# Kernel optimization log

Measured on AMD Instinct MI355X. Metric: run time of the kernel, lower is better.

The kernel has to match this reference:

```python
import jax, jax.numpy as jnp
from jax import lax
import numpy as np

K = 10            # size_feat
N_MU = 10         # number of mean-PSF components
NCH = K * K + N_MU  # 110 depthwise channels
KLEN = 65         # precomputed kernel length


def setup_inputs() -> dict:
    key = jax.random.key(0)
    ks = jax.random.split(key, 12)
    B, C, H, W = 1, 3, 256, 256
    img = jax.random.uniform(ks[0], (B, C, H, W), jnp.float32)
    zernike = jax.random.normal(ks[1], (B, H, W, 35), jnp.float32)
    # pos displacements (first 2 channels) scaled to a few pixels
    zernike = zernike.at[..., :2].multiply(2.0)
    fc1_w = jax.random.normal(ks[2], (200, 33), jnp.float32) / np.float32(np.sqrt(33))
    fc1_b = jax.random.normal(ks[3], (200,), jnp.float32) * 0.01
    fc2_w = jax.random.normal(ks[4], (200, 200), jnp.float32) / np.float32(np.sqrt(200))
    fc2_b = jax.random.normal(ks[5], (200,), jnp.float32) * 0.01
    fc3_w = jax.random.normal(ks[6], (100, 200), jnp.float32) * 0.01
    fc3_b = jnp.zeros((100,), jnp.float32)
    basis_left = jax.random.normal(ks[7], (KLEN, K), jnp.float32) * 0.05
    basis_right = jax.random.normal(ks[8], (KLEN, K), jnp.float32) * 0.05
    mu = jax.random.uniform(ks[9], (KLEN, N_MU), jnp.float32) / np.float32(KLEN)
    return dict(img=img, zernike=zernike, fc1_w=fc1_w, fc1_b=fc1_b,
                fc2_w=fc2_w, fc2_b=fc2_b, fc3_w=fc3_w, fc3_b=fc3_b,
                basis_left=basis_left, basis_right=basis_right, mu=mu, ksize=65)


def _grid_sample_border(img, pos):
    """Bilinear grid_sample, padding_mode='border', align_corners=False.
    img: (B,C,H,W), pos: (B,H,W,2) pixel displacements (x,y)."""
    B, C, H, W = img.shape
    yy, xx = jnp.meshgrid(jnp.arange(H, dtype=jnp.float32),
                          jnp.arange(W, dtype=jnp.float32), indexing='ij')
    grid = jnp.stack((xx, yy), -1)                       # (H,W,2)
    wh = jnp.array([W - 1, H - 1], jnp.float32)
    flow = 2.0 * (grid[None] + pos) / wh - 1.0           # (B,H,W,2) in [-1,1]
    ix = ((flow[..., 0] + 1.0) * W - 1.0) * 0.5
    iy = ((flow[..., 1] + 1.0) * H - 1.0) * 0.5
    ix = jnp.clip(ix, 0.0, W - 1)
    iy = jnp.clip(iy, 0.0, H - 1)
    x0 = jnp.floor(ix); y0 = jnp.floor(iy)
    wx = ix - x0;       wy = iy - y0
    x0i = jnp.clip(x0.astype(jnp.int32), 0, W - 1)
    y0i = jnp.clip(y0.astype(jnp.int32), 0, H - 1)
    x1i = jnp.clip(x0i + 1, 0, W - 1)
    y1i = jnp.clip(y0i + 1, 0, H - 1)

    def bilerp(im, x0i, x1i, y0i, y1i, wx, wy):
        g = lambda yi, xi: im[:, yi, xi]                 # (C,H,W)
        top = g(y0i, x0i) * (1 - wx) + g(y0i, x1i) * wx
        bot = g(y1i, x0i) * (1 - wx) + g(y1i, x1i) * wx
        return top * (1 - wy) + bot * wy

    return jax.vmap(bilerp)(img, x0i, x1i, y0i, y1i, wx, wy)


def _depthwise(x, w, pad_axis, pad):
    # x: (N, NCH, H, W); w: (NCH,1,kh,kw). Reflect 'same' padding on pad_axis.
    cfg = [(0, 0)] * 4
    cfg[pad_axis] = (pad, pad)
    xp = jnp.pad(x, cfg, mode='reflect')
    return lax.conv_general_dilated(
        xp, w, (1, 1), 'VALID',
        dimension_numbers=('NCHW', 'OIHW', 'NCHW'),
        feature_group_count=x.shape[1])


def _forward(img, zernike, fc1_w, fc1_b, fc2_w, fc2_b, fc3_w, fc3_b,
             basis_left, basis_right, mu, ksize):
    B, C, H, W = img.shape
    pad = ksize // 2
    # --- grid-sample warp ---
    tilt = _grid_sample_border(img, zernike[..., :2])    # (B,C,H,W)
    # --- per-pixel MLP -> PSF coefficients ---
    f = zernike[..., 2:]                                  # (B,H,W,33)
    h = jax.nn.leaky_relu(f @ fc1_w.T + fc1_b)
    h = jax.nn.leaky_relu(h @ fc2_w.T + fc2_b)
    coef = h @ fc3_w.T + fc3_b                            # (B,H,W,100)
    weight = jnp.concatenate(
        [coef, jnp.ones((B, H, W, N_MU), coef.dtype)], -1)  # (B,H,W,110)
    # --- elementwise weight multiply ---
    big = jnp.concatenate([tilt, jnp.ones_like(tilt)], 1)  # (B,2C,H,W)
    big = big[..., None] * weight[:, None]                 # (B,2C,H,W,110)
    x = big.reshape(B * 2 * C, H, W, NCH).transpose(0, 3, 1, 2)  # (B*2C,110,H,W)
    # --- separable depthwise blur kernels (outer products Z_i x X_j + mu) ---
    wl = jnp.concatenate([jnp.repeat(basis_left.T, K, axis=0), mu.T], 0)  # (110,klen)
    wr = jnp.concatenate([jnp.tile(basis_right.T, (K, 1)), mu.T], 0)      # (110,klen)
    wl = wl[:, None, :, None]                              # (110,1,klen,1)
    wr = wr[:, None, None, :]                              # (110,1,1,klen)
    y = _depthwise(x, wl, 2, pad)
    y = _depthwise(y, wr, 3, pad)
    d = y.reshape(B, 2 * C, NCH, H, W)
    out = jnp.sum(d[:, :3], axis=2) / jnp.sum(d[:, 3:], axis=2)  # (B,3,H,W)
    return out


def reference(img, zernike, fc1_w, fc1_b, fc2_w, fc2_b, fc3_w, fc3_b,
              basis_left, basis_right, mu, ksize):
    return _forward(img, zernike, fc1_w, fc1_b, fc2_w, fc2_b, fc3_w, fc3_b,
                    basis_left, basis_right, mu, ksize)
```

## Files before the change

kernel.cpp:

```cpp
#include <hip/hip_runtime.h>

#define HW 65536

typedef __attribute__((ext_vector_type(8))) short short8;
typedef __attribute__((ext_vector_type(4))) float float4v;

__device__ __forceinline__ int refl(int i){ if (i < 0) i = -i; if (i > 255) i = 510 - i; return i; }
__device__ __forceinline__ float lrelu(float x){ return x > 0.f ? x : 0.01f * x; }
__device__ __forceinline__ unsigned int f2bf(float x){
  union { float f; unsigned int u; } v; v.f = x;
  unsigned int r = v.u + 0x7fff + ((v.u >> 16) & 1);
  return r >> 16;
}
__device__ __forceinline__ unsigned int pk_bf16(float lo, float hi){
  unsigned int r;
  asm("v_cvt_pk_bf16_f32 %0, %1, %2" : "=v"(r) : "v"(lo), "v"(hi));
  return r;
}
__device__ __forceinline__ unsigned short f2h(float x){
  union { _Float16 h; unsigned short u; } v; v.h = (_Float16)x; return v.u;
}
__device__ __forceinline__ float h2f(unsigned short u){
  union { _Float16 h; unsigned short u; } v; v.u = u; return (float)v.h;
}

#define W2OFF 13312
#define W3OFF 59904
__global__ __launch_bounds__(256) void k_prep(const float* __restrict__ w1,
    const float* __restrict__ w2, const float* __restrict__ w3,
    const float* __restrict__ bl, const float* __restrict__ br,
    const float* __restrict__ mu, unsigned short* __restrict__ wbf,
    unsigned short* __restrict__ Tt, float* __restrict__ mucp){
  __shared__ float sm[650];
  __shared__ float sq[10];
  int bid = blockIdx.x;
  int tid = threadIdx.x;
  if (bid < 512){
    int i = bid * 256 + tid;
    if (i < 84992){
      if (i < 208 * 64){
        int n = i >> 6, k = i & 63;
        float v = (n < 200 && k < 33) ? w1[n * 33 + k] : 0.f;
        wbf[i] = (unsigned short)f2bf(v);
      } else if (i < W2OFF + 208 * 224){
        int j = i - W2OFF; int n = j / 224, k = j - n * 224;
        float v = (n < 200 && k < 200) ? w2[n * 200 + k] : 0.f;
        wbf[i] = (unsigned short)f2bf(v);
      } else {
        int j = i - W3OFF; int n = j / 224, k = j - n * 224;
        float v = (n < 100 && k < 200) ? w3[n * 200 + k] : 0.f;
        wbf[i] = (unsigned short)f2bf(v);
      }
    } else {
      int e = i - 84992;
      int t = e / 1536, rem = e - t * 1536;
      int m = rem / 96, k = rem - m * 96;
      int d = k - m;
      float v = 0.f;
      if (d >= 0 && d <= 64){
        if (t < 10)      v = bl[d * 10 + t];
        else if (t < 20) v = mu[d * 10 + (t - 10)];
        else             v = br[d * 10 + (t - 20)];
      }
      Tt[e] = (unsigned short)f2bf(v);
    }
  } else {
    for (int e = tid; e < 650; e += 256) sm[e] = mu[e];
    __syncthreads();
    if (tid < 10){
      float s = 0.f;
      for (int u = 0; u < 65; ++u) s += sm[u * 10 + tid];
      sq[tid] = s * s;
    }
    __syncthreads();
    if (tid == 0){
      float m = 0.f;
      #pragma unroll
      for (int mm = 0; mm < 10; ++mm) m += sq[mm];
      mucp[0] = m;
    }
  }
}

#define HSTR 232
#define BUFB 14848
__global__ __launch_bounds__(512) void k_mlp(const float* __restrict__ img,
    const float* __restrict__ zern,
    const float* __restrict__ b1f, const float* __restrict__ b2f,
    const float* __restrict__ b3f, const unsigned short* __restrict__ wbf,
    float* __restrict__ tilt, unsigned short* __restrict__ coefb){
  __shared__ char smem[2 * BUFB];
  unsigned short* H1  = (unsigned short*)smem;
  unsigned short* H3u = (unsigned short*)smem;
  unsigned short* XB  = (unsigned short*)(smem + BUFB);
  unsigned short* H2  = XB;
  int tid = threadIdx.x;
  int pix0 = blockIdx.x * 32;
  int lane = tid & 63, wv = tid >> 6;
  int ln = lane & 15, qd = lane >> 4;

  if (tid < 96){
    int m = tid & 31, c = tid >> 5;
    int pix = pix0 + m;
    int x = pix & 255, y = pix >> 8;
    float px = zern[pix * 35 + 0], py = zern[pix * 35 + 1];
    float ix = ((float)x + px) * (256.f / 255.f) - 0.5f;
    float iy = ((float)y + py) * (256.f / 255.f) - 0.5f;
    ix = fminf(fmaxf(ix, 0.f), 255.f);
    iy = fminf(fmaxf(iy, 0.f), 255.f);
    float x0f = floorf(ix), y0f = floorf(iy);
    float wx = ix - x0f, wy = iy - y0f;
    int x0 = (int)x0f, y0 = (int)y0f;
    int x1 = min(x0 + 1, 255), y1 = min(y0 + 1, 255);
    const float* im = img + c * HW;
    float g00 = im[y0 * 256 + x0], g01 = im[y0 * 256 + x1];
    float g10 = im[y1 * 256 + x0], g11 = im[y1 * 256 + x1];
    float top = g00 * (1.f - wx) + g01 * wx;
    float bot = g10 * (1.f - wx) + g11 * wx;
    tilt[c * HW + pix] = top * (1.f - wy) + bot * wy;
  }

  for (int e = tid; e < 1152; e += 512) ((int*)XB)[e] = 0;
  for (int e = tid; e < 384; e += 512){
    int m = e / 12, j = e - m * 12;
    ((int*)H1)[m * 116 + 104 + j] = 0;
  }
  __syncthreads();
  for (int e = tid; e < 32 * 33; e += 512){
    int m = e / 33, k = e - m * 33;
    XB[m * 72 + k] = (unsigned short)f2bf(zern[(pix0 + m) * 35 + 2 + k]);
  }
  __syncthreads();

  for (int nt = wv; nt < 13; nt += 8){
    int n = nt * 16 + ln;
    short8 b0 = *(const short8*)(wbf + n * 64 + qd * 8);
    short8 b1 = *(const short8*)(wbf + n * 64 + 32 + qd * 8);
    float bv = (n < 200) ? b1f[n] : 0.f;
    #pragma unroll
    for (int mt = 0; mt < 2; ++mt){
      float4v acc = {bv, bv, bv, bv};
      short8 a0 = *(const short8*)(XB + (mt * 16 + ln) * 72 + qd * 8);
      short8 a1 = *(const short8*)(XB + (mt * 16 + ln) * 72 + 32 + qd * 8);
      acc = __builtin_amdgcn_mfma_f32_16x16x32_bf16(a0, b0, acc, 0, 0, 0);
      acc = __builtin_amdgcn_mfma_f32_16x16x32_bf16(a1, b1, acc, 0, 0, 0);
      #pragma unroll
      for (int r = 0; r < 4; ++r)
        H1[(mt * 16 + qd * 4 + r) * HSTR + n] = (unsigned short)f2bf(lrelu(acc[r]));
    }
  }
  __syncthreads();

  for (int e = tid; e < 384; e += 512){
    int m = e / 12, j = e - m * 12;
    ((int*)H2)[m * 116 + 104 + j] = 0;
  }
  {
    const unsigned short* w2p = wbf + W2OFF;
    for (int nt = wv; nt < 13; nt += 8){
      int n = nt * 16 + ln;
      short8 bf[7];
      #pragma unroll
      for (int kc = 0; kc < 7; ++kc)
        bf[kc] = *(const short8*)(w2p + n * 224 + kc * 32 + qd * 8);
      float bv = (n < 200) ? b2f[n] : 0.f;
      #pragma unroll
      for (int mt = 0; mt < 2; ++mt){
        float4v acc = {bv, bv, bv, bv};
        #pragma unroll
        for (int kc = 0; kc < 7; ++kc){
          short8 af = *(const short8*)(H1 + (mt * 16 + ln) * HSTR + kc * 32 + qd * 8);
          acc = __builtin_amdgcn_mfma_f32_16x16x32_bf16(af, bf[kc], acc, 0, 0, 0);
        }
        #pragma unroll
        for (int r = 0; r < 4; ++r)
          H2[(mt * 16 + qd * 4 + r) * HSTR + n] = (unsigned short)f2bf(lrelu(acc[r]));
      }
    }
  }
  __syncthreads();

  {
    const unsigned short* w3p = wbf + W3OFF;
    for (int nt = wv; nt < 7; nt += 8){
      int n = nt * 16 + ln;
      short8 bf[7];
      #pragma unroll
      for (int kc = 0; kc < 7; ++kc)
        bf[kc] = *(const short8*)(w3p + n * 224 + kc * 32 + qd * 8);
      float bv = (n < 100) ? b3f[n] : 0.f;
      #pragma unroll
      for (int mt = 0; mt < 2; ++mt){
        float4v acc = {bv, bv, bv, bv};
        #pragma unroll
        for (int kc = 0; kc < 7; ++kc){
          short8 af = *(const short8*)(H2 + (mt * 16 + ln) * HSTR + kc * 32 + qd * 8);
          acc = __builtin_amdgcn_mfma_f32_16x16x32_bf16(af, bf[kc], acc, 0, 0, 0);
        }
        #pragma unroll
        for (int r = 0; r < 4; ++r)
          H3u[(mt * 16 + qd * 4 + r) * 113 + n] = f2h(acc[r]);
      }
    }
  }
  __syncthreads();

  for (int e = tid; e < 1600; e += 512){
    int n = e >> 4, mp = e & 15;
    unsigned int lo = H3u[(2 * mp) * 113 + n];
    unsigned int hi = H3u[(2 * mp + 1) * 113 + n];
    *(unsigned int*)(coefb + n * HW + pix0 + 2 * mp) = lo | (hi << 16);
  }
}

#define VB 344
__global__ __launch_bounds__(256) void k_vconv16(const float* __restrict__ tilt,
    const unsigned short* __restrict__ coefb, const unsigned short* __restrict__ Tt,
    unsigned short* __restrict__ sbuf, unsigned short* __restrict__ smu){
  __shared__ __align__(16) unsigned short sxb[2][16 * VB];
  int tid = threadIdx.x;
  int bid = blockIdx.x;
  int lane = tid & 63, wv = tid >> 6;
  int ln = lane & 15, qd = lane >> 4;
  int col = tid & 15, seg = tid >> 4;
  int r0 = seg * 20;

  int goff[20];
  #pragma unroll
  for (int q = 0; q < 20; ++q) goff[q] = refl(r0 + q - 32) * 256 + col;

  for (int e = tid; e < 768; e += 256){
    int b = e / 384, r = e - b * 384;
    int cc = r / 24, rp = r - cc * 24;
    sxb[b][cc * VB + 320 + rp] = 0;
  }

  if (bid < 640){
    int s = bid & 15;
    int cj = bid >> 4;
    int c = cj / 10, j = cj - c * 10;
    int x0 = s * 16;
    float treg[20];
    if (c < 3){
      const float* tc = tilt + c * HW + x0;
      #pragma unroll
      for (int q = 0; q < 20; ++q) treg[q] = tc[goff[q]];
    }
    unsigned short pf[20];
    {
      const unsigned short* cq = coefb + j * HW + x0;
      #pragma unroll
      for (int q = 0; q < 20; ++q) pf[q] = cq[goff[q]];
    }
    float4v acc[4];
    #pragma unroll
    for (int t = 0; t < 4; ++t) acc[t] = (float4v){0.f, 0.f, 0.f, 0.f};
    for (int i = 0; i < 10; ++i){
      int us = i & 1;
      unsigned short* sb = sxb[us];
      if (c < 3){
        #pragma unroll
        for (int q = 0; q < 10; ++q){
          float v0 = h2f(pf[2 * q]) * treg[2 * q];
          float v1 = h2f(pf[2 * q + 1]) * treg[2 * q + 1];
          *(unsigned int*)&sb[col * VB + r0 + 2 * q] = pk_bf16(v0, v1);
        }
      } else {
        #pragma unroll
        for (int q = 0; q < 10; ++q){
          *(unsigned int*)&sb[col * VB + r0 + 2 * q] = pk_bf16(h2f(pf[2 * q]), h2f(pf[2 * q + 1]));
        }
      }
      __syncthreads();
      if (i < 9){
        const unsigned short* cn = coefb + ((i + 1) * 10 + j) * HW + x0;
        #pragma unroll
        for (int q = 0; q < 20; ++q) pf[q] = cn[goff[q]];
      }
      const unsigned short* ta = Tt + i * 1536 + ln * 96 + qd * 8;
      short8 A0 = *(const short8*)(ta);
      short8 A1 = *(const short8*)(ta + 32);
      short8 A2 = *(const short8*)(ta + 64);
      #pragma unroll
      for (int t = 0; t < 4; ++t){
        int yt = wv * 4 + t;
        const unsigned short* bp = sb + ln * VB + yt * 16 + qd * 8;
        short8 B0 = *(const short8*)(bp);
        short8 B1 = *(const short8*)(bp + 32);
        short8 B2 = *(const short8*)(bp + 64);
        acc[t] = __builtin_amdgcn_mfma_f32_16x16x32_bf16(A0, B0, acc[t], 0, 0, 0);
        acc[t] = __builtin_amdgcn_mfma_f32_16x16x32_bf16(A1, B1, acc[t], 0, 0, 0);
        acc[t] = __builtin_amdgcn_mfma_f32_16x16x32_bf16(A2, B2, acc[t], 0, 0, 0);
      }
    }
    unsigned short* S = sbuf + (c * 10 + j) * HW + x0 + ln;
    #pragma unroll
    for (int t = 0; t < 4; ++t){
      int yt = wv * 4 + t;
      #pragma unroll
      for (int r = 0; r < 4; ++r)
        S[(yt * 16 + qd * 4 + r) * 256] = (unsigned short)f2bf(acc[t][r]);
    }
  } else {
    int b2 = bid - 640;
    int c = b2 >> 4, s = b2 & 15;
    int x0 = s * 16;
    const float* tc = tilt + c * HW + x0;
    float tv[20];
    #pragma unroll
    for (int q = 0; q < 20; ++q) tv[q] = tc[goff[q]];
    #pragma unroll
    for (int q = 0; q < 10; ++q){
      *(unsigned int*)&sxb[0][col * VB + r0 + 2 * q] = pk_bf16(tv[2 * q], tv[2 * q + 1]);
    }
    __syncthreads();
    for (int m = 0; m < 10; ++m){
      const unsigned short* ta = Tt + (10 + m) * 1536 + ln * 96 + qd * 8;
      short8 A0 = *(const short8*)(ta);
      short8 A1 = *(const short8*)(ta + 32);
      short8 A2 = *(const short8*)(ta + 64);
      float4v acc[4];
      #pragma unroll
      for (int t = 0; t < 4; ++t) acc[t] = (float4v){0.f, 0.f, 0.f, 0.f};
      #pragma unroll
      for (int t = 0; t < 4; ++t){
        int yt = wv * 4 + t;
        const unsigned short* bp = sxb[0] + ln * VB + yt * 16 + qd * 8;
        short8 B0 = *(const short8*)(bp);
        short8 B1 = *(const short8*)(bp + 32);
        short8 B2 = *(const short8*)(bp + 64);
        acc[t] = __builtin_amdgcn_mfma_f32_16x16x32_bf16(A0, B0, acc[t], 0, 0, 0);
        acc[t] = __builtin_amdgcn_mfma_f32_16x16x32_bf16(A1, B1, acc[t], 0, 0, 0);
        acc[t] = __builtin_amdgcn_mfma_f32_16x16x32_bf16(A2, B2, acc[t], 0, 0, 0);
      }
      unsigned short* S = smu + (c * 10 + m) * HW + x0 + ln;
      #pragma unroll
      for (int t = 0; t < 4; ++t){
        int yt = wv * 4 + t;
        #pragma unroll
        for (int r = 0; r < 4; ++r)
          S[(yt * 16 + qd * 4 + r) * 256] = (unsigned short)f2bf(acc[t][r]);
      }
    }
  }
}

#define HS2 344
__global__ __launch_bounds__(256) void k_hconv9(const unsigned short* __restrict__ sbuf,
    const unsigned short* __restrict__ smu, const unsigned short* __restrict__ Tt,
    float* __restrict__ part){
  __shared__ __align__(16) unsigned short sxb[16 * HS2];
  int tid = threadIdx.x;
  int grp = blockIdx.x >> 4;
  int yt  = blockIdx.x & 15;
  int y0 = yt * 16;
  int lane = tid & 63, wv = tid >> 6;
  int ln = lane & 15, qd = lane >> 4;
  int srow = tid >> 4, scol = tid & 15;
  int isbr = (grp < 8);
  int tgt, h;
  if (isbr){ tgt = grp >> 1; h = grp & 1; }
  else     { int g2 = grp - 8; tgt = g2 >> 1; h = g2 & 1; }
  const unsigned short* base = isbr ? (sbuf + tgt * 10 * HW) : (smu + tgt * 10 * HW);
  int tbase = isbr ? 20 : 10;

  for (int e = tid; e < 384; e += 256){
    int rr = e / 24, cp = e - rr * 24;
    sxb[rr * HS2 + 320 + cp] = 0;
  }

  int gx[20];
  #pragma unroll
  for (int q = 0; q < 20; ++q) gx[q] = refl(scol * 20 - 32 + q);

  float4v acc[4];
  #pragma unroll
  for (int t = 0; t < 4; ++t) acc[t] = (float4v){0.f, 0.f, 0.f, 0.f};

  for (int p = 0; p < 5; ++p){
    int col = h * 5 + p;
    const unsigned short* plane = base + col * HW + (y0 + srow) * 256;
    __syncthreads();
    unsigned short v[20];
    #pragma unroll
    for (int q = 0; q < 20; ++q) v[q] = plane[gx[q]];
    #pragma unroll
    for (int q = 0; q < 10; ++q){
      *(unsigned int*)&sxb[srow * HS2 + scol * 20 + 2 * q] =
          (unsigned int)v[2 * q] | ((unsigned int)v[2 * q + 1] << 16);
    }
    __syncthreads();
    const unsigned short* ta = Tt + (tbase + col) * 1536 + ln * 96 + qd * 8;
    short8 A0 = *(const short8*)(ta);
    short8 A1 = *(const short8*)(ta + 32);
    short8 A2 = *(const short8*)(ta + 64);
    #pragma unroll
    for (int t = 0; t < 4; ++t){
      int wt = wv * 4 + t;
      const unsigned short* bp = sxb + ln * HS2 + wt * 16 + qd * 8;
      short8 B0 = *(const short8*)(bp);
      short8 B1 = *(const short8*)(bp + 32);
      short8 B2 = *(const short8*)(bp + 64);
      acc[t] = __builtin_amdgcn_mfma_f32_16x16x32_bf16(A0, B0, acc[t], 0, 0, 0);
      acc[t] = __builtin_amdgcn_mfma_f32_16x16x32_bf16(A1, B1, acc[t], 0, 0, 0);
      acc[t] = __builtin_amdgcn_mfma_f32_16x16x32_bf16(A2, B2, acc[t], 0, 0, 0);
    }
  }
  #pragma unroll
  for (int t = 0; t < 4; ++t){
    int wt = wv * 4 + t;
    float4 res = {acc[t][0], acc[t][1], acc[t][2], acc[t][3]};
    *(float4*)(part + grp * HW + (y0 + ln) * 256 + wt * 16 + qd * 4) = res;
  }
}

__global__ __launch_bounds__(256) void k_final(const float* __restrict__ part,
                                               const float* __restrict__ mucp,
                                               float* __restrict__ out){
  int pix = blockIdx.x * 256 + threadIdx.x;
  float muC = mucp[0];
  float den = part[6 * HW + pix] + part[7 * HW + pix] + muC;
  float inv = 1.f / den;
  #pragma unroll
  for (int c = 0; c < 3; ++c){
    float num = part[(2 * c) * HW + pix] + part[(2 * c + 1) * HW + pix]
              + part[(8 + 2 * c) * HW + pix] + part[(9 + 2 * c) * HW + pix];
    out[c * HW + pix] = num * inv;
  }
}

extern "C" void kernel_launch(void* const* d_in, const int* in_sizes, int n_in,
                              void* d_out, int out_size, void* d_ws, size_t ws_size,
                              hipStream_t stream) {
  const float* img  = (const float*)d_in[0];
  const float* zern = (const float*)d_in[1];
  const float* w1   = (const float*)d_in[2];
  const float* b1   = (const float*)d_in[3];
  const float* w2   = (const float*)d_in[4];
  const float* b2   = (const float*)d_in[5];
  const float* w3   = (const float*)d_in[6];
  const float* b3   = (const float*)d_in[7];
  const float* bl   = (const float*)d_in[8];
  const float* br   = (const float*)d_in[9];
  const float* mu   = (const float*)d_in[10];
  float* out = (float*)d_out;

  float* w = (float*)d_ws;
  float* tilt = w;
  unsigned short* coefb = (unsigned short*)(w + 3 * HW);
  float* part = w + 3 * HW;
  unsigned short* sbuf = (unsigned short*)(w + 53 * HW);
  unsigned short* smu  = (unsigned short*)(w + 73 * HW);
  unsigned short* wbf  = (unsigned short*)(w + 53 * HW);
  unsigned short* Tt   = (unsigned short*)(w + 88 * HW);
  float* mucp = (float*)(Tt + 46080);

  k_prep<<<513, 256, 0, stream>>>(w1, w2, w3, bl, br, mu, wbf, Tt, mucp);
  k_mlp<<<2048, 512, 0, stream>>>(img, zern, b1, b2, b3, wbf, tilt, coefb);
  k_vconv16<<<688, 256, 0, stream>>>(tilt, coefb, Tt, sbuf, smu);
  k_hconv9<<<224, 256, 0, stream>>>(sbuf, smu, Tt, part);
  k_final<<<256, 256, 0, stream>>>(part, mucp, out);
}
```

Measured before the change: 149.2 us.

## Split vertical and horizontal conv kernels into more blocks for occupancy

The vertical conv kernel now splits each column strip into two 128-row halves, doubling the grid and halving per-block rows, accumulators and shared memory. The horizontal conv kernel no longer loops over the 5 planes per block; each plane gets its own block and writes a separate partial, and the final kernel sums 5x more partial planes. The aim is to fill more CUs on the GPU. The cost is more halo re-reads, extra partial-buffer traffic and more reads in the final reduction.

```diff
diff --git a/kernel.cpp b/kernel.cpp
--- a/kernel.cpp
+++ b/kernel.cpp
@@ -213,78 +213,81 @@
   }
 }
 
-#define VB 344
-__global__ __launch_bounds__(256) void k_vconv16(const float* __restrict__ tilt,
+#define VB2 216
+__global__ __launch_bounds__(256) void k_vconv17(const float* __restrict__ tilt,
     const unsigned short* __restrict__ coefb, const unsigned short* __restrict__ Tt,
     unsigned short* __restrict__ sbuf, unsigned short* __restrict__ smu){
-  __shared__ __align__(16) unsigned short sxb[2][16 * VB];
+  __shared__ __align__(16) unsigned short sxb[2][16 * VB2];
   int tid = threadIdx.x;
   int bid = blockIdx.x;
   int lane = tid & 63, wv = tid >> 6;
   int ln = lane & 15, qd = lane >> 4;
   int col = tid & 15, seg = tid >> 4;
-  int r0 = seg * 20;
-
-  int goff[20];
-  #pragma unroll
-  for (int q = 0; q < 20; ++q) goff[q] = refl(r0 + q - 32) * 256 + col;
+  int r0 = seg * 12;
 
   for (int e = tid; e < 768; e += 256){
     int b = e / 384, r = e - b * 384;
     int cc = r / 24, rp = r - cc * 24;
-    sxb[b][cc * VB + 320 + rp] = 0;
-  }
-
-  if (bid < 640){
+    sxb[b][cc * VB2 + 192 + rp] = 0;
+  }
+
+  if (bid < 1280){
     int s = bid & 15;
-    int cj = bid >> 4;
+    int yh = (bid >> 4) & 1;
+    int cj = bid >> 5;
     int c = cj / 10, j = cj - c * 10;
     int x0 = s * 16;
-    float treg[20];
+    int ybase = yh * 128;
+
+    int goff[12];
+    #pragma unroll
+    for (int q = 0; q < 12; ++q) goff[q] = refl(ybase + r0 + q - 32) * 256 + col;
+
+    float treg[12];
     if (c < 3){
       const float* tc = tilt + c * HW + x0;
       #pragma unroll
-      for (int q = 0; q < 20; ++q) treg[q] = tc[goff[q]];
-    }
-    unsigned short pf[20];
+      for (int q = 0; q < 12; ++q) treg[q] = tc[goff[q]];
+    }
+    unsigned short pf[12];
     {
       const unsigned short* cq = coefb + j * HW + x0;
       #pragma unroll
-      for (int q = 0; q < 20; ++q) pf[q] = cq[goff[q]];
-    }
-    float4v acc[4];
-    #pragma unroll
-    for (int t = 0; t < 4; ++t) acc[t] = (float4v){0.f, 0.f, 0.f, 0.f};
+      for (int q = 0; q < 12; ++q) pf[q] = cq[goff[q]];
+    }
+    float4v acc[2];
+    #pragma unroll
+    for (int t = 0; t < 2; ++t) acc[t] = (float4v){0.f, 0.f, 0.f, 0.f};
     for (int i = 0; i < 10; ++i){
       int us = i & 1;
       unsigned short* sb = sxb[us];
       if (c < 3){
         #pragma unroll
-        for (int q = 0; q < 10; ++q){
+        for (int q = 0; q < 6; ++q){
           float v0 = h2f(pf[2 * q]) * treg[2 * q];
           float v1 = h2f(pf[2 * q + 1]) * treg[2 * q + 1];
-          *(unsigned int*)&sb[col * VB + r0 + 2 * q] = pk_bf16(v0, v1);
+          *(unsigned int*)&sb[col * VB2 + r0 + 2 * q] = pk_bf16(v0, v1);
         }
       } else {
         #pragma unroll
-        for (int q = 0; q < 10; ++q){
-          *(unsigned int*)&sb[col * VB + r0 + 2 * q] = pk_bf16(h2f(pf[2 * q]), h2f(pf[2 * q + 1]));
+        for (int q = 0; q < 6; ++q){
+          *(unsigned int*)&sb[col * VB2 + r0 + 2 * q] = pk_bf16(h2f(pf[2 * q]), h2f(pf[2 * q + 1]));
         }
       }
       __syncthreads();
       if (i < 9){
         const unsigned short* cn = coefb + ((i + 1) * 10 + j) * HW + x0;
         #pragma unroll
-        for (int q = 0; q < 20; ++q) pf[q] = cn[goff[q]];
+        for (int q = 0; q < 12; ++q) pf[q] = cn[goff[q]];
       }
       const unsigned short* ta = Tt + i * 1536 + ln * 96 + qd * 8;
       short8 A0 = *(const short8*)(ta);
       short8 A1 = *(const short8*)(ta + 32);
       short8 A2 = *(const short8*)(ta + 64);
       #pragma unroll
-      for (int t = 0; t < 4; ++t){
-        int yt = wv * 4 + t;
-        const unsigned short* bp = sb + ln * VB + yt * 16 + qd * 8;
+      for (int t = 0; t < 2; ++t){
+        int yt = wv * 2 + t;
+        const unsigned short* bp = sb + ln * VB2 + yt * 16 + qd * 8;
         short8 B0 = *(const short8*)(bp);
         short8 B1 = *(const short8*)(bp + 32);
         short8 B2 = *(const short8*)(bp + 64);
@@ -295,23 +298,31 @@
     }
     unsigned short* S = sbuf + (c * 10 + j) * HW + x0 + ln;
     #pragma unroll
-    for (int t = 0; t < 4; ++t){
-      int yt = wv * 4 + t;
+    for (int t = 0; t < 2; ++t){
+      int yt = wv * 2 + t;
       #pragma unroll
       for (int r = 0; r < 4; ++r)
-        S[(yt * 16 + qd * 4 + r) * 256] = (unsigned short)f2bf(acc[t][r]);
+        S[(ybase + yt * 16 + qd * 4 + r) * 256] = (unsigned short)f2bf(acc[t][r]);
     }
   } else {
-    int b2 = bid - 640;
-    int c = b2 >> 4, s = b2 & 15;
+    int b2 = bid - 1280;
+    int c = b2 >> 5;
+    int r2 = b2 & 31;
+    int s = r2 >> 1, yh = r2 & 1;
     int x0 = s * 16;
+    int ybase = yh * 128;
+
+    int goff[12];
+    #pragma unroll
+    for (int q = 0; q < 12; ++q) goff[q] = refl(ybase + r0 + q - 32) * 256 + col;
+
     const float* tc = tilt + c * HW + x0;
-    float tv[20];
-    #pragma unroll
-    for (int q = 0; q < 20; ++q) tv[q] = tc[goff[q]];
-    #pragma unroll
-    for (int q = 0; q < 10; ++q){
-      *(unsigned int*)&sxb[0][col * VB + r0 + 2 * q] = pk_bf16(tv[2 * q], tv[2 * q + 1]);
+    float tv[12];
+    #pragma unroll
+    for (int q = 0; q < 12; ++q) tv[q] = tc[goff[q]];
+    #pragma unroll
+    for (int q = 0; q < 6; ++q){
+      *(unsigned int*)&sxb[0][col * VB2 + r0 + 2 * q] = pk_bf16(tv[2 * q], tv[2 * q + 1]);
     }
     __syncthreads();
     for (int m = 0; m < 10; ++m){
@@ -319,13 +330,13 @@
       short8 A0 = *(const short8*)(ta);
       short8 A1 = *(const short8*)(ta + 32);
       short8 A2 = *(const short8*)(ta + 64);
-      float4v acc[4];
-      #pragma unroll
-      for (int t = 0; t < 4; ++t) acc[t] = (float4v){0.f, 0.f, 0.f, 0.f};
-      #pragma unroll
-      for (int t = 0; t < 4; ++t){
-        int yt = wv * 4 + t;
-        const unsigned short* bp = sxb[0] + ln * VB + yt * 16 + qd * 8;
+      float4v acc[2];
+      #pragma unroll
+      for (int t = 0; t < 2; ++t) acc[t] = (float4v){0.f, 0.f, 0.f, 0.f};
+      #pragma unroll
+      for (int t = 0; t < 2; ++t){
+        int yt = wv * 2 + t;
+        const unsigned short* bp = sxb[0] + ln * VB2 + yt * 16 + qd * 8;
         short8 B0 = *(const short8*)(bp);
         short8 B1 = *(const short8*)(bp + 32);
         short8 B2 = *(const short8*)(bp + 64);
@@ -335,24 +346,27 @@
       }
       unsigned short* S = smu + (c * 10 + m) * HW + x0 + ln;
       #pragma unroll
-      for (int t = 0; t < 4; ++t){
-        int yt = wv * 4 + t;
+      for (int t = 0; t < 2; ++t){
+        int yt = wv * 2 + t;
         #pragma unroll
         for (int r = 0; r < 4; ++r)
-          S[(yt * 16 + qd * 4 + r) * 256] = (unsigned short)f2bf(acc[t][r]);
+          S[(ybase + yt * 16 + qd * 4 + r) * 256] = (unsigned short)f2bf(acc[t][r]);
       }
     }
   }
 }
 
 #define HS2 344
-__global__ __launch_bounds__(256) void k_hconv9(const unsigned short* __restrict__ sbuf,
+__global__ __launch_bounds__(256) void k_hconv10(const unsigned short* __restrict__ sbuf,
     const unsigned short* __restrict__ smu, const unsigned short* __restrict__ Tt,
     float* __restrict__ part){
   __shared__ __align__(16) unsigned short sxb[16 * HS2];
   int tid = threadIdx.x;
-  int grp = blockIdx.x >> 4;
-  int yt  = blockIdx.x & 15;
+  int bid = blockIdx.x;
+  int grp = bid / 80;
+  int rem = bid - grp * 80;
+  int yt = rem / 5;
+  int p  = rem - yt * 5;
   int y0 = yt * 16;
   int lane = tid & 63, wv = tid >> 6;
   int ln = lane & 15, qd = lane >> 4;
@@ -363,6 +377,7 @@
   else     { int g2 = grp - 8; tgt = g2 >> 1; h = g2 & 1; }
   const unsigned short* base = isbr ? (sbuf + tgt * 10 * HW) : (smu + tgt * 10 * HW);
   int tbase = isbr ? 20 : 10;
+  int col = h * 5 + p;
 
   for (int e = tid; e < 384; e += 256){
     int rr = e / 24, cp = e - rr * 24;
@@ -373,44 +388,34 @@
   #pragma unroll
   for (int q = 0; q < 20; ++q) gx[q] = refl(scol * 20 - 32 + q);
 
-  float4v acc[4];
-  #pragma unroll
-  for (int t = 0; t < 4; ++t) acc[t] = (float4v){0.f, 0.f, 0.f, 0.f};
-
-  for (int p = 0; p < 5; ++p){
-    int col = h * 5 + p;
-    const unsigned short* plane = base + col * HW + (y0 + srow) * 256;
-    __syncthreads();
-    unsigned short v[20];
-    #pragma unroll
-    for (int q = 0; q < 20; ++q) v[q] = plane[gx[q]];
-    #pragma unroll
-    for (int q = 0; q < 10; ++q){
-      *(unsigned int*)&sxb[srow * HS2 + scol * 20 + 2 * q] =
-          (unsigned int)v[2 * q] | ((unsigned int)v[2 * q + 1] << 16);
-    }
-    __syncthreads();
-    const unsigned short* ta = Tt + (tbase + col) * 1536 + ln * 96 + qd * 8;
-    short8 A0 = *(const short8*)(ta);
-    short8 A1 = *(const short8*)(ta + 32);
-    short8 A2 = *(const short8*)(ta + 64);
-    #pragma unroll
-    for (int t = 0; t < 4; ++t){
-      int wt = wv * 4 + t;
-      const unsigned short* bp = sxb + ln * HS2 + wt * 16 + qd * 8;
-      short8 B0 = *(const short8*)(bp);
-      short8 B1 = *(const short8*)(bp + 32);
-      short8 B2 = *(const short8*)(bp + 64);
-      acc[t] = __builtin_amdgcn_mfma_f32_16x16x32_bf16(A0, B0, acc[t], 0, 0, 0);
-      acc[t] = __builtin_amdgcn_mfma_f32_16x16x32_bf16(A1, B1, acc[t], 0, 0, 0);
-      acc[t] = __builtin_amdgcn_mfma_f32_16x16x32_bf16(A2, B2, acc[t], 0, 0, 0);
-    }
-  }
+  const unsigned short* plane = base + col * HW + (y0 + srow) * 256;
+  unsigned short v[20];
+  #pragma unroll
+  for (int q = 0; q < 20; ++q) v[q] = plane[gx[q]];
+  #pragma unroll
+  for (int q = 0; q < 10; ++q){
+    *(unsigned int*)&sxb[srow * HS2 + scol * 20 + 2 * q] =
+        (unsigned int)v[2 * q] | ((unsigned int)v[2 * q + 1] << 16);
+  }
+  __syncthreads();
+
+  const unsigned short* ta = Tt + (tbase + col) * 1536 + ln * 96 + qd * 8;
+  short8 A0 = *(const short8*)(ta);
+  short8 A1 = *(const short8*)(ta + 32);
+  short8 A2 = *(const short8*)(ta + 64);
   #pragma unroll
   for (int t = 0; t < 4; ++t){
     int wt = wv * 4 + t;
-    float4 res = {acc[t][0], acc[t][1], acc[t][2], acc[t][3]};
-    *(float4*)(part + grp * HW + (y0 + ln) * 256 + wt * 16 + qd * 4) = res;
+    float4v acc = {0.f, 0.f, 0.f, 0.f};
+    const unsigned short* bp = sxb + ln * HS2 + wt * 16 + qd * 8;
+    short8 B0 = *(const short8*)(bp);
+    short8 B1 = *(const short8*)(bp + 32);
+    short8 B2 = *(const short8*)(bp + 64);
+    acc = __builtin_amdgcn_mfma_f32_16x16x32_bf16(A0, B0, acc, 0, 0, 0);
+    acc = __builtin_amdgcn_mfma_f32_16x16x32_bf16(A1, B1, acc, 0, 0, 0);
+    acc = __builtin_amdgcn_mfma_f32_16x16x32_bf16(A2, B2, acc, 0, 0, 0);
+    float4 res = {acc[0], acc[1], acc[2], acc[3]};
+    *(float4*)(part + (grp * 5 + p) * HW + (y0 + ln) * 256 + wt * 16 + qd * 4) = res;
   }
 }
 
@@ -419,12 +424,20 @@
                                                float* __restrict__ out){
   int pix = blockIdx.x * 256 + threadIdx.x;
   float muC = mucp[0];
-  float den = part[6 * HW + pix] + part[7 * HW + pix] + muC;
-  float inv = 1.f / den;
+  float d = 0.f;
+  #pragma unroll
+  for (int g = 6; g < 8; ++g)
+    #pragma unroll
+    for (int p = 0; p < 5; ++p) d += part[(g * 5 + p) * HW + pix];
+  float inv = 1.f / (d + muC);
   #pragma unroll
   for (int c = 0; c < 3; ++c){
-    float num = part[(2 * c) * HW + pix] + part[(2 * c + 1) * HW + pix]
-              + part[(8 + 2 * c) * HW + pix] + part[(9 + 2 * c) * HW + pix];
+    float num = 0.f;
+    int gs[4] = {2 * c, 2 * c + 1, 8 + 2 * c, 9 + 2 * c};
+    #pragma unroll
+    for (int gi = 0; gi < 4; ++gi)
+      #pragma unroll
+      for (int p = 0; p < 5; ++p) num += part[(gs[gi] * 5 + p) * HW + pix];
     out[c * HW + pix] = num * inv;
   }
 }
@@ -448,16 +461,16 @@
   float* w = (float*)d_ws;
   float* tilt = w;
   unsigned short* coefb = (unsigned short*)(w + 3 * HW);
-  float* part = w + 3 * HW;
   unsigned short* sbuf = (unsigned short*)(w + 53 * HW);
   unsigned short* smu  = (unsigned short*)(w + 73 * HW);
   unsigned short* wbf  = (unsigned short*)(w + 53 * HW);
   unsigned short* Tt   = (unsigned short*)(w + 88 * HW);
   float* mucp = (float*)(Tt + 46080);
+  float* part = w + 93 * HW;
 
   k_prep<<<513, 256, 0, stream>>>(w1, w2, w3, bl, br, mu, wbf, Tt, mucp);
   k_mlp<<<2048, 512, 0, stream>>>(img, zern, b1, b2, b3, wbf, tilt, coefb);
-  k_vconv16<<<688, 256, 0, stream>>>(tilt, coefb, Tt, sbuf, smu);
-  k_hconv9<<<224, 256, 0, stream>>>(sbuf, smu, Tt, part);
+  k_vconv17<<<1376, 256, 0, stream>>>(tilt, coefb, Tt, sbuf, smu);
+  k_hconv10<<<1120, 256, 0, stream>>>(sbuf, smu, Tt, part);
   k_final<<<256, 256, 0, stream>>>(part, mucp, out);
 }
```

Result: slower. 165.0 us (+10.6%).
